# Optimization experiments

Hardware: AMD Instinct MI355X
Metric: run time of the kernel (lower is better)

## Reference

```python
import jax, jax.numpy as jnp
import numpy as np

D_MODEL = 512


def setup_inputs() -> dict:
    key = jax.random.key(0)
    ks = jax.random.split(key, 9)
    B, S, D = 2, 4096, D_MODEL
    scale = 1.0 / np.sqrt(D)
    return {
        "Q": jax.random.normal(ks[0], (B, S, D), dtype=jnp.float32),
        "K": jax.random.normal(ks[1], (B, S, D), dtype=jnp.float32),
        "V": jax.random.normal(ks[2], (B, S, D), dtype=jnp.float32),
        "W_q": jax.random.normal(ks[3], (D, D), dtype=jnp.float32) * scale,
        "b_q": jax.random.normal(ks[4], (D,), dtype=jnp.float32) * scale,
        "W_k": jax.random.normal(ks[5], (D, D), dtype=jnp.float32) * scale,
        "b_k": jax.random.normal(ks[6], (D,), dtype=jnp.float32) * scale,
        "W_v": jax.random.normal(ks[7], (D, D), dtype=jnp.float32) * scale,
        "b_v": jax.random.normal(ks[8], (D,), dtype=jnp.float32) * scale,
    }


def reference(Q, K, V, W_q, b_q, W_k, b_k, W_v, b_v):
    # Linear projections (torch Linear: x @ W.T + b)
    q = jnp.einsum("bsd,ed->bse", Q, W_q) + b_q  # [B,S,D]
    k = jnp.einsum("bsd,ed->bse", K, W_k) + b_k
    v = jnp.einsum("bsd,ed->bse", V, W_v) + b_v
    d_k = k.shape[-1]
    scores = jnp.einsum("bqd,bkd->bqk", q, k) / jnp.sqrt(jnp.asarray(d_k, q.dtype))
    attn = jax.nn.softmax(scores, axis=-1)  # [B,S,S]
    return jnp.einsum("bqk,bkd->bqd", attn, v)
```

## Files before the change

kernel.cpp:

```cpp
#include <hip/hip_runtime.h>
#include <hip/hip_bf16.h>
#include <math.h>
#include <stdint.h>

typedef __attribute__((ext_vector_type(8))) short short8;
typedef __attribute__((ext_vector_type(4))) float floatx4;
typedef __attribute__((ext_vector_type(4))) unsigned short ushort4v;

__device__ __forceinline__ void gload_lds16(const void* g, void* lds) {
    __builtin_amdgcn_global_load_lds(
        (__attribute__((address_space(1))) void*)(g),
        (__attribute__((address_space(3))) void*)(lds), 16, 0, 0);
}
__device__ __forceinline__ float bf16bits_to_f(unsigned short u) {
    union { unsigned int i; float f; } x; x.i = ((unsigned int)u) << 16; return x.f;
}
__device__ __forceinline__ unsigned short f_to_bf16bits(float f) {
    union { float f; unsigned int i; } x; x.f = f;
    unsigned int lsb = (x.i >> 16) & 1u;
    x.i += 0x7fffu + lsb;
    return (unsigned short)(x.i >> 16);
}

__global__ __launch_bounds__(256) void conv1_kernel(
    const float4* __restrict__ in, ushort4v* __restrict__ out)
{
    const int i = blockIdx.x * 256 + threadIdx.x;
    float4 v = in[i];
    ushort4v o;
    o[0] = f_to_bf16bits(v.x); o[1] = f_to_bf16bits(v.y);
    o[2] = f_to_bf16bits(v.z); o[3] = f_to_bf16bits(v.w);
    out[i] = o;
}

__global__ __launch_bounds__(256) void conv_wb_kernel(
    const float* __restrict__ Wq, const float* __restrict__ Wk, const float* __restrict__ Wv,
    const float* __restrict__ bq, const float* __restrict__ bk, const float* __restrict__ bv,
    unsigned short* __restrict__ Wo,
    unsigned short* __restrict__ bo)
{
    const int m = blockIdx.y;
    const float* W = (m == 0) ? Wq : (m == 1) ? Wk : Wv;
    const float* b = (m == 0) ? bq : (m == 1) ? bk : bv;
    if (blockIdx.x < 256) {
        const int idx = (blockIdx.x * 256 + threadIdx.x) * 4;
        float4 v = *(const float4*)&W[idx];
        ushort4v o;
        o[0] = f_to_bf16bits(v.x); o[1] = f_to_bf16bits(v.y);
        o[2] = f_to_bf16bits(v.z); o[3] = f_to_bf16bits(v.w);
        *(ushort4v*)&Wo[(size_t)m * 262144 + idx] = o;
    } else if (threadIdx.x < 128) {
        const int idx = threadIdx.x * 4;
        float4 v = *(const float4*)&b[idx];
        ushort4v o;
        o[0] = f_to_bf16bits(v.x); o[1] = f_to_bf16bits(v.y);
        o[2] = f_to_bf16bits(v.z); o[3] = f_to_bf16bits(v.w);
        *(ushort4v*)&bo[(size_t)m * 512 + idx] = o;
    }
}

__global__ __launch_bounds__(256, 2) void proj_kernel(
    const unsigned short* __restrict__ X,
    const unsigned short* __restrict__ W,
    const unsigned short* __restrict__ bias,
    unsigned short* __restrict__ qbuf,
    unsigned short* __restrict__ kbuf,
    unsigned short* __restrict__ vTbuf,
    int mode, float qscale)
{
    __shared__ __align__(16) unsigned short Xs[128 * 64];
    __shared__ __align__(16) unsigned short Ws[128 * 64];

    const int tid = threadIdx.x;
    const int wave = tid >> 6, lane = tid & 63, quad = lane >> 4, l15 = lane & 15;
    const int m0 = (int)(blockIdx.x >> 2) << 7;
    const int n0 = (int)(blockIdx.x & 3) << 7;
    const int mw = (wave >> 1) << 6, nw = (wave & 1) << 6;

    floatx4 acc[4][4];
    #pragma unroll
    for (int i = 0; i < 4; i++)
        #pragma unroll
        for (int j = 0; j < 4; j++) acc[i][j] = floatx4{0.f, 0.f, 0.f, 0.f};

    for (int kt = 0; kt < 512; kt += 64) {
        #pragma unroll
        for (int i = 0; i < 4; i++) {
            const int r0 = wave * 32 + i * 8;
            gload_lds16(X + (size_t)(m0 + r0 + (lane >> 3)) * 512 + kt + (lane & 7) * 8, &Xs[r0 * 64]);
            gload_lds16(W + (size_t)(n0 + r0 + (lane >> 3)) * 512 + kt + (lane & 7) * 8, &Ws[r0 * 64]);
        }
        __syncthreads();
        #pragma unroll
        for (int kk = 0; kk < 64; kk += 32) {
            short8 a[4], b[4];
            #pragma unroll
            for (int i = 0; i < 4; i++) a[i] = *(const short8*)&Xs[(mw + 16 * i + l15) * 64 + kk + quad * 8];
            #pragma unroll
            for (int j = 0; j < 4; j++) b[j] = *(const short8*)&Ws[(nw + 16 * j + l15) * 64 + kk + quad * 8];
            #pragma unroll
            for (int i = 0; i < 4; i++)
                #pragma unroll
                for (int j = 0; j < 4; j++)
                    acc[i][j] = __builtin_amdgcn_mfma_f32_16x16x32_bf16(a[i], b[j], acc[i][j], 0, 0, 0);
        }
        __syncthreads();
    }

    float bfj[4];
    #pragma unroll
    for (int j = 0; j < 4; j++) bfj[j] = bf16bits_to_f(bias[n0 + nw + 16 * j + l15]);

    if (mode < 2) {
        unsigned short* out = (mode == 0) ? qbuf : kbuf;
        const float s = (mode == 0) ? qscale : 1.0f;
        #pragma unroll
        for (int i = 0; i < 4; i++) {
            const int mrow = m0 + mw + 16 * i + quad * 4;
            #pragma unroll
            for (int j = 0; j < 4; j++) {
                const int n = n0 + nw + 16 * j + l15;
                #pragma unroll
                for (int r = 0; r < 4; r++)
                    out[(size_t)(mrow + r) * 512 + n] = f_to_bf16bits((acc[i][j][r] + bfj[j]) * s);
            }
        }
    } else {
        #pragma unroll
        for (int i = 0; i < 4; i++) {
            const int mrow = m0 + mw + 16 * i + quad * 4;
            const int bb = mrow >> 12;
            const int s4 = mrow & 4095;
            #pragma unroll
            for (int j = 0; j < 4; j++) {
                const int n = n0 + nw + 16 * j + l15;
                ushort4v pk;
                #pragma unroll
                for (int r = 0; r < 4; r++) pk[r] = f_to_bf16bits(acc[i][j][r] + bfj[j]);
                *(ushort4v*)&vTbuf[((size_t)bb * 512 + n) * 4096 + s4] = pk;
            }
        }
    }
}

template <int NSPLIT>
__global__ __launch_bounds__(256, 2) void attn_kernel(
    const unsigned short* __restrict__ q,
    const unsigned short* __restrict__ k,
    const unsigned short* __restrict__ vT,
    unsigned short* __restrict__ num,
    float* __restrict__ denom)
{
    constexpr int TK  = 32;
    constexpr int KST = 520;
    constexpr int PST = 40;
    __shared__ __align__(16) unsigned short Ks [TK * KST];
    __shared__ __align__(16) unsigned short Vts[512 * TK];
    __shared__ __align__(16) unsigned short Ps [64 * PST];

    const int tid = threadIdx.x;
    const int wave = tid >> 6, lane = tid & 63, quad = lane >> 4, l15 = lane & 15;
    const int bid = blockIdx.x;
    const int sp   = bid & (NSPLIT - 1);
    const int qblk = bid / NSPLIT;
    const int bb = qblk >> 6;
    const int q0 = (qblk & 63) << 6;
    const size_t rowbase = (size_t)bb * 4096 + q0;

    short8 qf[16];
    {
        const unsigned short* qrow = q + (rowbase + 16 * wave + l15) * 512;
        #pragma unroll
        for (int t = 0; t < 16; t++) qf[t] = *(const short8*)&qrow[t * 32 + quad * 8];
    }

    floatx4 oacc[4][8];
    #pragma unroll
    for (int i = 0; i < 4; i++)
        #pragma unroll
        for (int c = 0; c < 8; c++) oacc[i][c] = floatx4{0.f, 0.f, 0.f, 0.f};
    float dsum[4] = {0.f, 0.f, 0.f, 0.f};

    const unsigned short* kb = k  + (size_t)bb * 4096 * 512;
    const unsigned short* vb = vT + (size_t)bb * 512 * 4096;

    const int jbeg = sp * (4096 / NSPLIT);
    const int jend = jbeg + (4096 / NSPLIT);
    for (int j0 = jbeg; j0 < jend; j0 += TK) {
        #pragma unroll
        for (int r = 0; r < 8; r++) {
            const int row = wave * 8 + r;
            gload_lds16(kb + (size_t)(j0 + row) * 512 + lane * 8, &Ks[row * KST]);
        }
        #pragma unroll
        for (int i2 = 0; i2 < 8; i2++) {
            const int dd0 = (wave * 8 + i2) * 16;
            gload_lds16(vb + (size_t)(dd0 + (lane >> 2)) * 4096 + j0 + (lane & 3) * 8,
                        &Vts[dd0 * TK]);
        }
        __syncthreads();

        floatx4 sA[2], sB[2];
        sA[0] = sA[1] = sB[0] = sB[1] = floatx4{0.f, 0.f, 0.f, 0.f};
        #pragma unroll
        for (int t = 0; t < 16; t += 2) {
            #pragma unroll
            for (int c = 0; c < 2; c++) {
                short8 b0 = *(const short8*)&Ks[(c * 16 + l15) * KST + t * 32 + quad * 8];
                sA[c] = __builtin_amdgcn_mfma_f32_16x16x32_bf16(qf[t], b0, sA[c], 0, 0, 0);
                short8 b1 = *(const short8*)&Ks[(c * 16 + l15) * KST + (t + 1) * 32 + quad * 8];
                sB[c] = __builtin_amdgcn_mfma_f32_16x16x32_bf16(qf[t + 1], b1, sB[c], 0, 0, 0);
            }
        }
        #pragma unroll
        for (int c = 0; c < 2; c++) {
            #pragma unroll
            for (int r = 0; r < 4; r++) {
                const float p = __expf(fminf(sA[c][r] + sB[c][r], 30.0f));
                const unsigned short pb = f_to_bf16bits(p);
                dsum[r] += bf16bits_to_f(pb);
                Ps[(16 * wave + quad * 4 + r) * PST + c * 16 + l15] = pb;
            }
        }
        __syncthreads();

        short8 ap[4];
        #pragma unroll
        for (int i = 0; i < 4; i++) ap[i] = *(const short8*)&Ps[(16 * i + l15) * PST + quad * 8];
        #pragma unroll
        for (int c = 0; c < 8; c++) {
            short8 bvf = *(const short8*)&Vts[(128 * wave + 16 * c + l15) * TK + quad * 8];
            #pragma unroll
            for (int i = 0; i < 4; i++)
                oacc[i][c] = __builtin_amdgcn_mfma_f32_16x16x32_bf16(ap[i], bvf, oacc[i][c], 0, 0, 0);
        }
        __syncthreads();
    }

    #pragma unroll
    for (int r = 0; r < 4; r++) {
        float v = dsum[r];
        v += __shfl_xor(v, 1);
        v += __shfl_xor(v, 2);
        v += __shfl_xor(v, 4);
        v += __shfl_xor(v, 8);
        dsum[r] = v;
    }
    if (l15 == 0) {
        #pragma unroll
        for (int r = 0; r < 4; r++)
            denom[(size_t)sp * 8192 + rowbase + 16 * wave + quad * 4 + r] = dsum[r];
    }

    #pragma unroll
    for (int i = 0; i < 4; i++) {
        #pragma unroll
        for (int r = 0; r < 4; r++) {
            const size_t row = rowbase + 16 * i + quad * 4 + r;
            unsigned short* np_ = num + ((size_t)sp * 8192 + row) * 512 + 128 * wave + l15;
            #pragma unroll
            for (int c = 0; c < 8; c++)
                np_[16 * c] = f_to_bf16bits(oacc[i][c][r]);
        }
    }
}

__global__ __launch_bounds__(256) void combine_kernel(
    const unsigned short* __restrict__ num,
    const float* __restrict__ denom,
    float* __restrict__ out,
    int nsplit)
{
    const int gid = blockIdx.x * 256 + threadIdx.x;
    const int srow = gid >> 6;
    const int d0 = (gid & 63) << 3;
    float s[8];
    #pragma unroll
    for (int e = 0; e < 8; e++) s[e] = 0.f;
    float den = 0.f;
    for (int sp = 0; sp < nsplit; sp++) {
        den += denom[(size_t)sp * 8192 + srow];
        short8 v = *(const short8*)(num + ((size_t)sp * 8192 + srow) * 512 + d0);
        #pragma unroll
        for (int e = 0; e < 8; e++) s[e] += bf16bits_to_f((unsigned short)v[e]);
    }
    const float inv = 1.0f / den;
    float4 o0, o1;
    o0.x = s[0] * inv; o0.y = s[1] * inv; o0.z = s[2] * inv; o0.w = s[3] * inv;
    o1.x = s[4] * inv; o1.y = s[5] * inv; o1.z = s[6] * inv; o1.w = s[7] * inv;
    float* op = out + (size_t)srow * 512 + d0;
    *(float4*)op = o0;
    *(float4*)(op + 4) = o1;
}

extern "C" void kernel_launch(void* const* d_in, const int* in_sizes, int n_in,
                              void* d_out, int out_size, void* d_ws, size_t ws_size,
                              hipStream_t stream)
{
    (void)in_sizes; (void)n_in; (void)out_size;
    const float* Qin = (const float*)d_in[0];
    const float* Kin = (const float*)d_in[1];
    const float* Vin = (const float*)d_in[2];
    const float* Wq  = (const float*)d_in[3];
    const float* bq  = (const float*)d_in[4];
    const float* Wk  = (const float*)d_in[5];
    const float* bk  = (const float*)d_in[6];
    const float* Wv  = (const float*)d_in[7];
    const float* bv  = (const float*)d_in[8];

    const size_t M  = (size_t)8192 * 512;
    const size_t WS = (size_t)512 * 512;

    auto need = [&](size_t a_elems, int ns) -> size_t {
        return 2 * (a_elems + 3 * M + 3 * WS + 3 * 512) + 16 + (size_t)ns * 8192 * 4;
    };
    int nsplit; size_t a_elems; bool batched;
    if (ws_size >= need(4 * M, 4))      { nsplit = 4; a_elems = 4 * M; batched = true;  }
    else if (ws_size >= need(3 * M, 2)) { nsplit = 2; a_elems = 3 * M; batched = true;  }
    else                                { nsplit = 1; a_elems = 1 * M; batched = false; }

    unsigned short* ws   = (unsigned short*)d_ws;
    unsigned short* slotA = ws;
    unsigned short* qbuf  = ws + a_elems;
    unsigned short* kbuf  = qbuf + M;
    unsigned short* vTbuf = kbuf + M;
    unsigned short* Wc    = vTbuf + M;
    unsigned short* bc    = Wc + 3 * WS;
    size_t denom_off = (2 * (size_t)((bc + 3 * 512) - ws) + 15) & ~(size_t)15;
    float* denom = (float*)((char*)d_ws + denom_off);
    unsigned short* numb = slotA;

    const float qscale = 1.0f / sqrtf(512.0f);
    const float* Xin[3] = { Qin, Kin, Vin };

    conv_wb_kernel<<<dim3(257, 3), 256, 0, stream>>>(Wq, Wk, Wv, bq, bk, bv, Wc, bc);

    if (batched) {
        for (int m = 0; m < 3; m++)
            conv1_kernel<<<4096, 256, 0, stream>>>((const float4*)Xin[m],
                                                   (ushort4v*)(slotA + (size_t)m * M));
        for (int m = 0; m < 3; m++)
            proj_kernel<<<256, 256, 0, stream>>>(slotA + (size_t)m * M,
                                                 Wc + (size_t)m * WS, bc + (size_t)m * 512,
                                                 qbuf, kbuf, vTbuf, m, qscale);
    } else {
        for (int m = 0; m < 3; m++) {
            conv1_kernel<<<4096, 256, 0, stream>>>((const float4*)Xin[m], (ushort4v*)slotA);
            proj_kernel<<<256, 256, 0, stream>>>(slotA,
                                                 Wc + (size_t)m * WS, bc + (size_t)m * 512,
                                                 qbuf, kbuf, vTbuf, m, qscale);
        }
    }

    if (nsplit == 4)
        attn_kernel<4><<<dim3(512), dim3(256), 0, stream>>>(qbuf, kbuf, vTbuf, numb, denom);
    else if (nsplit == 2)
        attn_kernel<2><<<dim3(256), dim3(256), 0, stream>>>(qbuf, kbuf, vTbuf, numb, denom);
    else
        attn_kernel<1><<<dim3(128), dim3(256), 0, stream>>>(qbuf, kbuf, vTbuf, numb, denom);

    combine_kernel<<<dim3(2048), dim3(256), 0, stream>>>(
        numb, denom, (float*)d_out, nsplit);
}
```

Baseline: 265.5 us.

## Fuse fp32-to-bf16 conversion into projection GEMM and batch three projections

Removes the separate conversion kernels for inputs and weights. The projection kernel now loads fp32 X and W directly, converts them to bf16 in registers and writes them to LDS, and a single launch with grid.y=3 covers all three projections. This removes an extra round trip of the converted activations through global memory and several kernel launches. In exchange, each block now re-reads and re-converts fp32 weights, the direct-to-LDS async loads are replaced by register-staged loads, and the loop is restructured to use a single barrier per iteration.

After: 286.7 us. 8.0% more time.

```diff
diff --git a/kernel.cpp b/kernel.cpp
--- a/kernel.cpp
+++ b/kernel.cpp
@@ -21,55 +21,30 @@
     x.i += 0x7fffu + lsb;
     return (unsigned short)(x.i >> 16);
 }
-
-__global__ __launch_bounds__(256) void conv1_kernel(
-    const float4* __restrict__ in, ushort4v* __restrict__ out)
-{
-    const int i = blockIdx.x * 256 + threadIdx.x;
-    float4 v = in[i];
+__device__ __forceinline__ ushort4v cvt4(float4 v) {
     ushort4v o;
     o[0] = f_to_bf16bits(v.x); o[1] = f_to_bf16bits(v.y);
     o[2] = f_to_bf16bits(v.z); o[3] = f_to_bf16bits(v.w);
-    out[i] = o;
-}
-
-__global__ __launch_bounds__(256) void conv_wb_kernel(
-    const float* __restrict__ Wq, const float* __restrict__ Wk, const float* __restrict__ Wv,
-    const float* __restrict__ bq, const float* __restrict__ bk, const float* __restrict__ bv,
-    unsigned short* __restrict__ Wo,
-    unsigned short* __restrict__ bo)
-{
-    const int m = blockIdx.y;
-    const float* W = (m == 0) ? Wq : (m == 1) ? Wk : Wv;
-    const float* b = (m == 0) ? bq : (m == 1) ? bk : bv;
-    if (blockIdx.x < 256) {
-        const int idx = (blockIdx.x * 256 + threadIdx.x) * 4;
-        float4 v = *(const float4*)&W[idx];
-        ushort4v o;
-        o[0] = f_to_bf16bits(v.x); o[1] = f_to_bf16bits(v.y);
-        o[2] = f_to_bf16bits(v.z); o[3] = f_to_bf16bits(v.w);
-        *(ushort4v*)&Wo[(size_t)m * 262144 + idx] = o;
-    } else if (threadIdx.x < 128) {
-        const int idx = threadIdx.x * 4;
-        float4 v = *(const float4*)&b[idx];
-        ushort4v o;
-        o[0] = f_to_bf16bits(v.x); o[1] = f_to_bf16bits(v.y);
-        o[2] = f_to_bf16bits(v.z); o[3] = f_to_bf16bits(v.w);
-        *(ushort4v*)&bo[(size_t)m * 512 + idx] = o;
-    }
-}
-
-__global__ __launch_bounds__(256, 2) void proj_kernel(
-    const unsigned short* __restrict__ X,
-    const unsigned short* __restrict__ W,
-    const unsigned short* __restrict__ bias,
+    return o;
+}
+
+__global__ __launch_bounds__(256, 2) void proj_fused_kernel(
+    const float* __restrict__ Qin, const float* __restrict__ Kin, const float* __restrict__ Vin,
+    const float* __restrict__ Wq, const float* __restrict__ bq,
+    const float* __restrict__ Wk, const float* __restrict__ bk,
+    const float* __restrict__ Wv, const float* __restrict__ bv,
     unsigned short* __restrict__ qbuf,
     unsigned short* __restrict__ kbuf,
     unsigned short* __restrict__ vTbuf,
-    int mode, float qscale)
+    float qscale)
 {
     __shared__ __align__(16) unsigned short Xs[128 * 64];
     __shared__ __align__(16) unsigned short Ws[128 * 64];
+
+    const int mode = blockIdx.y;
+    const float* X    = (mode == 0) ? Qin : (mode == 1) ? Kin : Vin;
+    const float* W    = (mode == 0) ? Wq  : (mode == 1) ? Wk  : Wv;
+    const float* bias = (mode == 0) ? bq  : (mode == 1) ? bk  : bv;
 
     const int tid = threadIdx.x;
     const int wave = tid >> 6, lane = tid & 63, quad = lane >> 4, l15 = lane & 15;
@@ -77,6 +52,12 @@
     const int n0 = (int)(blockIdx.x & 3) << 7;
     const int mw = (wave >> 1) << 6, nw = (wave & 1) << 6;
 
+    const int srow = tid >> 1, sseg = tid & 1;
+    const float* xrow = X + (size_t)(m0 + srow) * 512 + sseg * 32;
+    const float* wrow = W + (size_t)(n0 + srow) * 512 + sseg * 32;
+    unsigned short* xls = &Xs[srow * 64 + sseg * 32];
+    unsigned short* wls = &Ws[srow * 64 + sseg * 32];
+
     floatx4 acc[4][4];
     #pragma unroll
     for (int i = 0; i < 4; i++)
@@ -84,11 +65,17 @@
         for (int j = 0; j < 4; j++) acc[i][j] = floatx4{0.f, 0.f, 0.f, 0.f};
 
     for (int kt = 0; kt < 512; kt += 64) {
-        #pragma unroll
-        for (int i = 0; i < 4; i++) {
-            const int r0 = wave * 32 + i * 8;
-            gload_lds16(X + (size_t)(m0 + r0 + (lane >> 3)) * 512 + kt + (lane & 7) * 8, &Xs[r0 * 64]);
-            gload_lds16(W + (size_t)(n0 + r0 + (lane >> 3)) * 512 + kt + (lane & 7) * 8, &Ws[r0 * 64]);
+        float4 xv[8], wv[8];
+        #pragma unroll
+        for (int i = 0; i < 8; i++) {
+            xv[i] = *(const float4*)(xrow + kt + i * 4);
+            wv[i] = *(const float4*)(wrow + kt + i * 4);
+        }
+        __syncthreads();
+        #pragma unroll
+        for (int i = 0; i < 8; i++) {
+            *(ushort4v*)(xls + i * 4) = cvt4(xv[i]);
+            *(ushort4v*)(wls + i * 4) = cvt4(wv[i]);
         }
         __syncthreads();
         #pragma unroll
@@ -104,12 +91,11 @@
                 for (int j = 0; j < 4; j++)
                     acc[i][j] = __builtin_amdgcn_mfma_f32_16x16x32_bf16(a[i], b[j], acc[i][j], 0, 0, 0);
         }
-        __syncthreads();
     }
 
     float bfj[4];
     #pragma unroll
-    for (int j = 0; j < 4; j++) bfj[j] = bf16bits_to_f(bias[n0 + nw + 16 * j + l15]);
+    for (int j = 0; j < 4; j++) bfj[j] = bias[n0 + nw + 16 * j + l15];
 
     if (mode < 2) {
         unsigned short* out = (mode == 0) ? qbuf : kbuf;
@@ -308,56 +294,31 @@
     const float* Wv  = (const float*)d_in[7];
     const float* bv  = (const float*)d_in[8];
 
-    const size_t M  = (size_t)8192 * 512;
-    const size_t WS = (size_t)512 * 512;
-
-    auto need = [&](size_t a_elems, int ns) -> size_t {
-        return 2 * (a_elems + 3 * M + 3 * WS + 3 * 512) + 16 + (size_t)ns * 8192 * 4;
+    const size_t M = (size_t)8192 * 512;
+
+    auto need = [&](size_t ns) -> size_t {
+        return ((size_t)ns + 3) * M * 2 + (size_t)ns * 8192 * 4 + 64;
     };
-    int nsplit; size_t a_elems; bool batched;
-    if (ws_size >= need(4 * M, 4))      { nsplit = 4; a_elems = 4 * M; batched = true;  }
-    else if (ws_size >= need(3 * M, 2)) { nsplit = 2; a_elems = 3 * M; batched = true;  }
-    else                                { nsplit = 1; a_elems = 1 * M; batched = false; }
+    const int nsplit = (ws_size >= need(4)) ? 4 : (ws_size >= need(2)) ? 2 : 1;
 
     unsigned short* ws   = (unsigned short*)d_ws;
-    unsigned short* slotA = ws;
-    unsigned short* qbuf  = ws + a_elems;
-    unsigned short* kbuf  = qbuf + M;
-    unsigned short* vTbuf = kbuf + M;
-    unsigned short* Wc    = vTbuf + M;
-    unsigned short* bc    = Wc + 3 * WS;
-    size_t denom_off = (2 * (size_t)((bc + 3 * 512) - ws) + 15) & ~(size_t)15;
-    float* denom = (float*)((char*)d_ws + denom_off);
-    unsigned short* numb = slotA;
+    unsigned short* numb = ws;
+    unsigned short* qs   = ws + (size_t)nsplit * M;
+    unsigned short* ks   = qs + M;
+    unsigned short* vT   = ks + M;
+    float* denom = (float*)(((uintptr_t)(vT + M) + 15) & ~(uintptr_t)15);
 
     const float qscale = 1.0f / sqrtf(512.0f);
-    const float* Xin[3] = { Qin, Kin, Vin };
-
-    conv_wb_kernel<<<dim3(257, 3), 256, 0, stream>>>(Wq, Wk, Wv, bq, bk, bv, Wc, bc);
-
-    if (batched) {
-        for (int m = 0; m < 3; m++)
-            conv1_kernel<<<4096, 256, 0, stream>>>((const float4*)Xin[m],
-                                                   (ushort4v*)(slotA + (size_t)m * M));
-        for (int m = 0; m < 3; m++)
-            proj_kernel<<<256, 256, 0, stream>>>(slotA + (size_t)m * M,
-                                                 Wc + (size_t)m * WS, bc + (size_t)m * 512,
-                                                 qbuf, kbuf, vTbuf, m, qscale);
-    } else {
-        for (int m = 0; m < 3; m++) {
-            conv1_kernel<<<4096, 256, 0, stream>>>((const float4*)Xin[m], (ushort4v*)slotA);
-            proj_kernel<<<256, 256, 0, stream>>>(slotA,
-                                                 Wc + (size_t)m * WS, bc + (size_t)m * 512,
-                                                 qbuf, kbuf, vTbuf, m, qscale);
-        }
-    }
+
+    proj_fused_kernel<<<dim3(256, 3), dim3(256), 0, stream>>>(
+        Qin, Kin, Vin, Wq, bq, Wk, bk, Wv, bv, qs, ks, vT, qscale);
 
     if (nsplit == 4)
-        attn_kernel<4><<<dim3(512), dim3(256), 0, stream>>>(qbuf, kbuf, vTbuf, numb, denom);
+        attn_kernel<4><<<dim3(512), dim3(256), 0, stream>>>(qs, ks, vT, numb, denom);
     else if (nsplit == 2)
-        attn_kernel<2><<<dim3(256), dim3(256), 0, stream>>>(qbuf, kbuf, vTbuf, numb, denom);
+        attn_kernel<2><<<dim3(256), dim3(256), 0, stream>>>(qs, ks, vT, numb, denom);
     else
-        attn_kernel<1><<<dim3(128), dim3(256), 0, stream>>>(qbuf, kbuf, vTbuf, numb, denom);
+        attn_kernel<1><<<dim3(128), dim3(256), 0, stream>>>(qs, ks, vT, numb, denom);
 
     combine_kernel<<<dim3(2048), dim3(256), 0, stream>>>(
         numb, denom, (float*)d_out, nsplit);
```

## Load V fragments directly to registers and batch conversion and projection launches

Applied to the files above, without the earlier changes.

The attention kernel now reads V^T fragments straight from global memory into registers instead of staging them through LDS. This removes the V LDS buffer and the trailing barrier of each key tile. The three input-conversion launches are merged into one kernel, and the three projection GEMMs run as a single launch with a grid y dimension. An 8-way key split is also added for when the workspace is large enough. The risks are less-coalesced global loads for V with exposed latency, and a larger partial-numerator workspace plus heavier combine work when nsplit is 8.

After: 259.9 us. 1.02x faster.

```diff
diff --git a/kernel.cpp b/kernel.cpp
--- a/kernel.cpp
+++ b/kernel.cpp
@@ -22,15 +22,30 @@
     return (unsigned short)(x.i >> 16);
 }
 
-__global__ __launch_bounds__(256) void conv1_kernel(
-    const float4* __restrict__ in, ushort4v* __restrict__ out)
-{
-    const int i = blockIdx.x * 256 + threadIdx.x;
-    float4 v = in[i];
+__global__ __launch_bounds__(256) void conv_qkv_kernel(
+    const float* __restrict__ Q, const float* __restrict__ K, const float* __restrict__ V,
+    unsigned short* __restrict__ out)
+{
+    const int seg = blockIdx.x >> 12;
+    const int blk = blockIdx.x & 4095;
+    const float* src = (seg == 0) ? Q : (seg == 1) ? K : V;
+    const int idx = (blk * 256 + threadIdx.x) * 4;
+    float4 v = *(const float4*)&src[idx];
     ushort4v o;
     o[0] = f_to_bf16bits(v.x); o[1] = f_to_bf16bits(v.y);
     o[2] = f_to_bf16bits(v.z); o[3] = f_to_bf16bits(v.w);
-    out[i] = o;
+    *(ushort4v*)&out[(size_t)seg * 4194304 + idx] = o;
+}
+
+__global__ __launch_bounds__(256) void conv1_kernel(
+    const float* __restrict__ in, unsigned short* __restrict__ out)
+{
+    const int idx = (blockIdx.x * 256 + threadIdx.x) * 4;
+    float4 v = *(const float4*)&in[idx];
+    ushort4v o;
+    o[0] = f_to_bf16bits(v.x); o[1] = f_to_bf16bits(v.y);
+    o[2] = f_to_bf16bits(v.z); o[3] = f_to_bf16bits(v.w);
+    *(ushort4v*)&out[idx] = o;
 }
 
 __global__ __launch_bounds__(256) void conv_wb_kernel(
@@ -60,16 +75,22 @@
 }
 
 __global__ __launch_bounds__(256, 2) void proj_kernel(
-    const unsigned short* __restrict__ X,
-    const unsigned short* __restrict__ W,
-    const unsigned short* __restrict__ bias,
+    const unsigned short* __restrict__ Xall,
+    size_t xstride, int mode_base,
+    const unsigned short* __restrict__ Wall,
+    const unsigned short* __restrict__ ball,
     unsigned short* __restrict__ qbuf,
     unsigned short* __restrict__ kbuf,
     unsigned short* __restrict__ vTbuf,
-    int mode, float qscale)
+    float qscale)
 {
     __shared__ __align__(16) unsigned short Xs[128 * 64];
     __shared__ __align__(16) unsigned short Ws[128 * 64];
+
+    const int mode = mode_base + blockIdx.y;
+    const unsigned short* X = Xall + (size_t)blockIdx.y * xstride;
+    const unsigned short* W = Wall + (size_t)mode * 262144;
+    const unsigned short* bias = ball + (size_t)mode * 512;
 
     const int tid = threadIdx.x;
     const int wave = tid >> 6, lane = tid & 63, quad = lane >> 4, l15 = lane & 15;
@@ -154,9 +175,8 @@
     constexpr int TK  = 32;
     constexpr int KST = 520;
     constexpr int PST = 40;
-    __shared__ __align__(16) unsigned short Ks [TK * KST];
-    __shared__ __align__(16) unsigned short Vts[512 * TK];
-    __shared__ __align__(16) unsigned short Ps [64 * PST];
+    __shared__ __align__(16) unsigned short Ks[TK * KST];
+    __shared__ __align__(16) unsigned short Ps[64 * PST];
 
     const int tid = threadIdx.x;
     const int wave = tid >> 6, lane = tid & 63, quad = lane >> 4, l15 = lane & 15;
@@ -182,7 +202,8 @@
     float dsum[4] = {0.f, 0.f, 0.f, 0.f};
 
     const unsigned short* kb = k  + (size_t)bb * 4096 * 512;
-    const unsigned short* vb = vT + (size_t)bb * 512 * 4096;
+    const unsigned short* vrow = vT + (size_t)bb * 512 * 4096
+                               + (size_t)(128 * wave + l15) * 4096 + quad * 8;
 
     const int jbeg = sp * (4096 / NSPLIT);
     const int jend = jbeg + (4096 / NSPLIT);
@@ -192,13 +213,12 @@
             const int row = wave * 8 + r;
             gload_lds16(kb + (size_t)(j0 + row) * 512 + lane * 8, &Ks[row * KST]);
         }
-        #pragma unroll
-        for (int i2 = 0; i2 < 8; i2++) {
-            const int dd0 = (wave * 8 + i2) * 16;
-            gload_lds16(vb + (size_t)(dd0 + (lane >> 2)) * 4096 + j0 + (lane & 3) * 8,
-                        &Vts[dd0 * TK]);
-        }
         __syncthreads();
+
+        short8 vf[8];
+        #pragma unroll
+        for (int c = 0; c < 8; c++)
+            vf[c] = *(const short8*)&vrow[(size_t)c * 16 * 4096 + j0];
 
         floatx4 sA[2], sB[2];
         sA[0] = sA[1] = sB[0] = sB[1] = floatx4{0.f, 0.f, 0.f, 0.f};
@@ -229,12 +249,10 @@
         for (int i = 0; i < 4; i++) ap[i] = *(const short8*)&Ps[(16 * i + l15) * PST + quad * 8];
         #pragma unroll
         for (int c = 0; c < 8; c++) {
-            short8 bvf = *(const short8*)&Vts[(128 * wave + 16 * c + l15) * TK + quad * 8];
             #pragma unroll
             for (int i = 0; i < 4; i++)
-                oacc[i][c] = __builtin_amdgcn_mfma_f32_16x16x32_bf16(ap[i], bvf, oacc[i][c], 0, 0, 0);
-        }
-        __syncthreads();
+                oacc[i][c] = __builtin_amdgcn_mfma_f32_16x16x32_bf16(ap[i], vf[c], oacc[i][c], 0, 0, 0);
+        }
     }
 
     #pragma unroll
@@ -308,56 +326,53 @@
     const float* Wv  = (const float*)d_in[7];
     const float* bv  = (const float*)d_in[8];
 
-    const size_t M  = (size_t)8192 * 512;
-    const size_t WS = (size_t)512 * 512;
-
-    auto need = [&](size_t a_elems, int ns) -> size_t {
-        return 2 * (a_elems + 3 * M + 3 * WS + 3 * 512) + 16 + (size_t)ns * 8192 * 4;
+    const size_t M   = (size_t)8192 * 512;
+    const size_t WS_ = (size_t)512 * 512;
+
+    auto need = [&](size_t sa, int ns) -> size_t {
+        return (sa + 3 * M) * 2 + 3 * WS_ * 2 + 3 * 512 * 2 + 64 + (size_t)ns * 8192 * 4;
     };
-    int nsplit; size_t a_elems; bool batched;
-    if (ws_size >= need(4 * M, 4))      { nsplit = 4; a_elems = 4 * M; batched = true;  }
-    else if (ws_size >= need(3 * M, 2)) { nsplit = 2; a_elems = 3 * M; batched = true;  }
-    else                                { nsplit = 1; a_elems = 1 * M; batched = false; }
-
-    unsigned short* ws   = (unsigned short*)d_ws;
+    int nsplit; size_t sa; bool batched;
+    if      (ws_size >= need(8 * M, 8)) { nsplit = 8; sa = 8 * M; batched = true; }
+    else if (ws_size >= need(4 * M, 4)) { nsplit = 4; sa = 4 * M; batched = true; }
+    else if (ws_size >= need(3 * M, 2)) { nsplit = 2; sa = 3 * M; batched = true; }
+    else                                { nsplit = 1; sa = 1 * M; batched = false; }
+
+    unsigned short* ws    = (unsigned short*)d_ws;
     unsigned short* slotA = ws;
-    unsigned short* qbuf  = ws + a_elems;
-    unsigned short* kbuf  = qbuf + M;
-    unsigned short* vTbuf = kbuf + M;
-    unsigned short* Wc    = vTbuf + M;
-    unsigned short* bc    = Wc + 3 * WS;
-    size_t denom_off = (2 * (size_t)((bc + 3 * 512) - ws) + 15) & ~(size_t)15;
-    float* denom = (float*)((char*)d_ws + denom_off);
+    unsigned short* qs    = ws + sa;
+    unsigned short* ks    = qs + M;
+    unsigned short* vT    = ks + M;
+    unsigned short* Wc    = vT + M;
+    unsigned short* bc    = Wc + 3 * WS_;
+    float* denom = (float*)(((uintptr_t)(bc + 3 * 512) + 15) & ~(uintptr_t)15);
     unsigned short* numb = slotA;
 
     const float qscale = 1.0f / sqrtf(512.0f);
-    const float* Xin[3] = { Qin, Kin, Vin };
-
-    conv_wb_kernel<<<dim3(257, 3), 256, 0, stream>>>(Wq, Wk, Wv, bq, bk, bv, Wc, bc);
+
+    conv_wb_kernel<<<dim3(257, 3), dim3(256), 0, stream>>>(Wq, Wk, Wv, bq, bk, bv, Wc, bc);
 
     if (batched) {
-        for (int m = 0; m < 3; m++)
-            conv1_kernel<<<4096, 256, 0, stream>>>((const float4*)Xin[m],
-                                                   (ushort4v*)(slotA + (size_t)m * M));
-        for (int m = 0; m < 3; m++)
-            proj_kernel<<<256, 256, 0, stream>>>(slotA + (size_t)m * M,
-                                                 Wc + (size_t)m * WS, bc + (size_t)m * 512,
-                                                 qbuf, kbuf, vTbuf, m, qscale);
+        conv_qkv_kernel<<<dim3(3 * 4096), dim3(256), 0, stream>>>(Qin, Kin, Vin, slotA);
+        proj_kernel<<<dim3(256, 3), dim3(256), 0, stream>>>(
+            slotA, M, 0, Wc, bc, qs, ks, vT, qscale);
     } else {
+        const float* Xin[3] = { Qin, Kin, Vin };
         for (int m = 0; m < 3; m++) {
-            conv1_kernel<<<4096, 256, 0, stream>>>((const float4*)Xin[m], (ushort4v*)slotA);
-            proj_kernel<<<256, 256, 0, stream>>>(slotA,
-                                                 Wc + (size_t)m * WS, bc + (size_t)m * 512,
-                                                 qbuf, kbuf, vTbuf, m, qscale);
-        }
-    }
-
-    if (nsplit == 4)
-        attn_kernel<4><<<dim3(512), dim3(256), 0, stream>>>(qbuf, kbuf, vTbuf, numb, denom);
+            conv1_kernel<<<dim3(4096), dim3(256), 0, stream>>>(Xin[m], slotA);
+            proj_kernel<<<dim3(256, 1), dim3(256), 0, stream>>>(
+                slotA, 0, m, Wc, bc, qs, ks, vT, qscale);
+        }
+    }
+
+    if (nsplit == 8)
+        attn_kernel<8><<<dim3(1024), dim3(256), 0, stream>>>(qs, ks, vT, numb, denom);
+    else if (nsplit == 4)
+        attn_kernel<4><<<dim3(512), dim3(256), 0, stream>>>(qs, ks, vT, numb, denom);
     else if (nsplit == 2)
-        attn_kernel<2><<<dim3(256), dim3(256), 0, stream>>>(qbuf, kbuf, vTbuf, numb, denom);
+        attn_kernel<2><<<dim3(256), dim3(256), 0, stream>>>(qs, ks, vT, numb, denom);
     else
-        attn_kernel<1><<<dim3(128), dim3(256), 0, stream>>>(qbuf, kbuf, vTbuf, numb, denom);
+        attn_kernel<1><<<dim3(128), dim3(256), 0, stream>>>(qs, ks, vT, numb, denom);
 
     combine_kernel<<<dim3(2048), dim3(256), 0, stream>>>(
         numb, denom, (float*)d_out, nsplit);
```
